# Kernel optimization log

Measured on AMD Instinct MI355X. Metric: run time of the kernel, lower is better.

The kernel has to match this reference:

```python
import jax, jax.numpy as jnp
import numpy as np
from jax import lax

WINDOW_SIZE = 11
SIGMA = 1.5
LEVELS = 5
WEIGHTS = jnp.array([0.0448, 0.2856, 0.3001, 0.2363, 0.1333], dtype=jnp.float32)


def _make_window(ws, channel):
    # 1D gaussian, sigma=1.5, normalized; outer product -> 2D window, tiled per channel
    x = jnp.arange(ws, dtype=jnp.float32) - ws // 2
    g = jnp.exp(-(x * x) / (2.0 * SIGMA * SIGMA))
    g = g / g.sum()
    w2 = jnp.outer(g, g)  # [ws, ws]
    return jnp.broadcast_to(w2[None, None], (channel, 1, ws, ws))


def _dwconv(x, win, channel):
    # depthwise VALID conv, matches F.conv2d(..., padding=0, groups=channel)
    return lax.conv_general_dilated(
        x, win, window_strides=(1, 1), padding='VALID',
        feature_group_count=channel,
        dimension_numbers=('NCHW', 'OIHW', 'NCHW'))


def _ssim_cs(img1, img2):
    # dynamic data range, as in the torch source (L=1 for [0,1) inputs)
    max_val = jnp.where(jnp.max(img1) > 128.0, 255.0, 1.0)
    min_val = jnp.where(jnp.min(img1) < -0.5, -1.0, 0.0)
    L = max_val - min_val

    n, c, h, w = img1.shape
    ws = min(WINDOW_SIZE, h, w)  # static python int
    win = _make_window(ws, c)

    mu1 = _dwconv(img1, win, c)
    mu2 = _dwconv(img2, win, c)
    mu1_sq = mu1 * mu1
    mu2_sq = mu2 * mu2
    mu1_mu2 = mu1 * mu2
    sigma1_sq = _dwconv(img1 * img1, win, c) - mu1_sq
    sigma2_sq = _dwconv(img2 * img2, win, c) - mu2_sq
    sigma12 = _dwconv(img1 * img2, win, c) - mu1_mu2

    C1 = (0.01 * L) ** 2
    C2 = (0.03 * L) ** 2
    v1 = 2.0 * sigma12 + C2
    v2 = sigma1_sq + sigma2_sq + C2
    cs = jnp.mean(v1 / v2)
    ssim_map = (2.0 * mu1_mu2 + C1) * v1 / ((mu1_sq + mu2_sq + C1) * v2)
    return jnp.mean(ssim_map), cs


def _avg_pool2(x):
    # F.avg_pool2d(x, (2,2)): stride 2, no padding (floors odd dims)
    n, c, h, w = x.shape
    x = x[:, :, : (h // 2) * 2, : (w // 2) * 2]
    return x.reshape(n, c, h // 2, 2, w // 2, 2).mean(axis=(3, 5))


def setup_inputs() -> dict:
    key = jax.random.key(0)
    k1, k2 = jax.random.split(key)
    img1 = jax.random.uniform(k1, (16, 3, 512, 512), dtype=jnp.float32)
    img2 = jax.random.uniform(k2, (16, 3, 512, 512), dtype=jnp.float32)
    return {"img1": img1, "img2": img2}


def reference(img1, img2):
    mssim, mcs = [], []
    for _ in range(LEVELS):  # fixed 5-level pyramid, shapes shrink each level
        s, c = _ssim_cs(img1, img2)
        mssim.append(s)
        mcs.append(c)
        img1 = _avg_pool2(img1)
        img2 = _avg_pool2(img2)
    mssim = (jnp.stack(mssim) + 1.0) / 2.0  # normalize=True
    mcs = (jnp.stack(mcs) + 1.0) / 2.0
    pow1 = mcs ** WEIGHTS
    pow2 = mssim ** WEIGHTS
    # NOTE: faithful to source: prod over (pow1[:-1] * pow2[-1]) broadcasts pow2[-1]
    return jnp.prod(pow1[:-1] * pow2[-1])
```

## Files before the change

### kernel.cpp

```cpp
#include <hip/hip_runtime.h>


#define NTHR 512

typedef float v4  __attribute__((ext_vector_type(4)));
typedef float v2f __attribute__((ext_vector_type(2)));

__device__ __forceinline__ float frcp(float x) { return __builtin_amdgcn_rcpf(x); }

#define GW_DEF const float GW[11] = {0.00102840f, 0.00759877f, 0.03600070f, \
    0.10936069f, 0.21300636f, 0.26601172f, 0.21300636f, 0.10936069f,        \
    0.03600070f, 0.00759877f, 0.00102840f};

__device__ __forceinline__ void conv11(const float* s, const float* d,
                                       v4& hs, v4& hd, v4& hss, v4& hdd)
{
    GW_DEF
    #pragma unroll
    for (int j = 0; j < 11; ++j) {
        float w = GW[j];
        v4 sv = {s[j], s[j+1], s[j+2], s[j+3]};
        v4 dv = {d[j], d[j+1], d[j+2], d[j+3]};
        v4 wsv = w * sv, wdv = w * dv;
        hs += wsv; hd += wdv; hss += wsv * sv; hdd += wdv * dv;
    }
}

template<int TROWS>
__device__ void hpass_direct(const float* __restrict__ p1, const float* __restrict__ p2,
                             int H, int tx0, int ty0, v4* hb)
{
    constexpr int HR = TROWS + 10;
    for (int task = threadIdx.x; task < HR * 4; task += NTHR) {
        const int r = task >> 2, cg = task & 3;
        const int gr = ty0 + r;
        const int c0 = tx0 + cg * 8;
        v4 hsA = 0.f, hdA = 0.f, hssA = 0.f, hddA = 0.f;
        v4 hsB = 0.f, hdB = 0.f, hssB = 0.f, hddB = 0.f;
        if (gr < H) {
            float s[20], d[20];
            if (c0 + 20 <= H) {
                const float* pa = p1 + (size_t)gr * H + c0;
                const float* pb = p2 + (size_t)gr * H + c0;
                v4 va0 = *(const v4*)(pa);
                v4 va1 = *(const v4*)(pa + 4);
                v4 va2 = *(const v4*)(pa + 8);
                v4 va3 = *(const v4*)(pa + 12);
                v4 va4 = *(const v4*)(pa + 16);
                v4 vb0 = *(const v4*)(pb);
                v4 vb1 = *(const v4*)(pb + 4);
                v4 vb2 = *(const v4*)(pb + 8);
                v4 vb3 = *(const v4*)(pb + 12);
                v4 vb4 = *(const v4*)(pb + 16);
                v4 sv0 = va0 + vb0, dv0 = va0 - vb0;
                v4 sv1 = va1 + vb1, dv1 = va1 - vb1;
                v4 sv2 = va2 + vb2, dv2 = va2 - vb2;
                v4 sv3 = va3 + vb3, dv3 = va3 - vb3;
                v4 sv4 = va4 + vb4, dv4 = va4 - vb4;
                s[0]=sv0.x; s[1]=sv0.y; s[2]=sv0.z; s[3]=sv0.w;
                s[4]=sv1.x; s[5]=sv1.y; s[6]=sv1.z; s[7]=sv1.w;
                s[8]=sv2.x; s[9]=sv2.y; s[10]=sv2.z; s[11]=sv2.w;
                s[12]=sv3.x; s[13]=sv3.y; s[14]=sv3.z; s[15]=sv3.w;
                s[16]=sv4.x; s[17]=sv4.y; s[18]=sv4.z; s[19]=sv4.w;
                d[0]=dv0.x; d[1]=dv0.y; d[2]=dv0.z; d[3]=dv0.w;
                d[4]=dv1.x; d[5]=dv1.y; d[6]=dv1.z; d[7]=dv1.w;
                d[8]=dv2.x; d[9]=dv2.y; d[10]=dv2.z; d[11]=dv2.w;
                d[12]=dv3.x; d[13]=dv3.y; d[14]=dv3.z; d[15]=dv3.w;
                d[16]=dv4.x; d[17]=dv4.y; d[18]=dv4.z; d[19]=dv4.w;
            } else {
                #pragma unroll
                for (int q = 0; q < 20; ++q) {
                    int cc = c0 + q;
                    float a = (cc < H) ? p1[(size_t)gr * H + cc] : 0.f;
                    float b = (cc < H) ? p2[(size_t)gr * H + cc] : 0.f;
                    s[q] = a + b; d[q] = a - b;
                }
            }
            GW_DEF
            #pragma unroll
            for (int j = 0; j < 11; ++j) {
                float w = GW[j];
                v4 svA = {s[j],   s[j+1], s[j+2], s[j+3]};
                v4 dvA = {d[j],   d[j+1], d[j+2], d[j+3]};
                v4 svB = {s[j+4], s[j+5], s[j+6], s[j+7]};
                v4 dvB = {d[j+4], d[j+5], d[j+6], d[j+7]};
                v4 wsA = w * svA, wdA = w * dvA;
                v4 wsB = w * svB, wdB = w * dvB;
                hsA += wsA; hdA += wdA; hssA += wsA * svA; hddA += wdA * dvA;
                hsB += wsB; hdB += wdB; hssB += wsB * svB; hddB += wdB * dvB;
            }
        }
        v4* row = &hb[r * 33 + cg * 8];
        row[0] = (v4){hsA.x, hdA.x, hssA.x, hddA.x};
        row[1] = (v4){hsA.y, hdA.y, hssA.y, hddA.y};
        row[2] = (v4){hsA.z, hdA.z, hssA.z, hddA.z};
        row[3] = (v4){hsA.w, hdA.w, hssA.w, hddA.w};
        row[4] = (v4){hsB.x, hdB.x, hssB.x, hddB.x};
        row[5] = (v4){hsB.y, hdB.y, hssB.y, hddB.y};
        row[6] = (v4){hsB.z, hdB.z, hssB.z, hddB.z};
        row[7] = (v4){hsB.w, hdB.w, hssB.w, hddB.w};
    }
}

__device__ __forceinline__ float pool2g(const float* __restrict__ sp, int SD, int gr, int cc)
{
    const float* q = sp + (size_t)(4 * gr) * SD + 4 * cc;
    v4 r0 = *(const v4*)q;
    v4 r1 = *(const v4*)(q + SD);
    v4 r2 = *(const v4*)(q + 2 * SD);
    v4 r3 = *(const v4*)(q + 3 * SD);
    float a00 = 0.25f * ((r0.x + r0.y) + (r1.x + r1.y));
    float a01 = 0.25f * ((r0.z + r0.w) + (r1.z + r1.w));
    float a10 = 0.25f * ((r2.x + r2.y) + (r3.x + r3.y));
    float a11 = 0.25f * ((r2.z + r2.w) + (r3.z + r3.w));
    return 0.25f * ((a00 + a01) + (a10 + a11));
}

__device__ __forceinline__ float pool3g(const float* __restrict__ sp, int SD, int gr, int cc)
{
    const float* q = sp + (size_t)(8 * gr) * SD + 8 * cc;
    float p2h[2][2];
    #pragma unroll
    for (int h = 0; h < 2; ++h) {
        const float* qq = q + (size_t)(4 * h) * SD;
        v4 A0 = *(const v4*)qq;
        v4 A1 = *(const v4*)(qq + SD);
        v4 A2 = *(const v4*)(qq + 2 * SD);
        v4 A3 = *(const v4*)(qq + 3 * SD);
        v4 B0 = *(const v4*)(qq + 4);
        v4 B1 = *(const v4*)(qq + SD + 4);
        v4 B2 = *(const v4*)(qq + 2 * SD + 4);
        v4 B3 = *(const v4*)(qq + 3 * SD + 4);
        float p00 = 0.25f * ((A0.x + A0.y) + (A1.x + A1.y));
        float p01 = 0.25f * ((A0.z + A0.w) + (A1.z + A1.w));
        float p10 = 0.25f * ((A2.x + A2.y) + (A3.x + A3.y));
        float p11 = 0.25f * ((A2.z + A2.w) + (A3.z + A3.w));
        float q00 = 0.25f * ((B0.x + B0.y) + (B1.x + B1.y));
        float q01 = 0.25f * ((B0.z + B0.w) + (B1.z + B1.w));
        float q10 = 0.25f * ((B2.x + B2.y) + (B3.x + B3.y));
        float q11 = 0.25f * ((B2.z + B2.w) + (B3.z + B3.w));
        p2h[h][0] = 0.25f * ((p00 + p01) + (p10 + p11));
        p2h[h][1] = 0.25f * ((q00 + q01) + (q10 + q11));
    }
    return 0.25f * ((p2h[0][0] + p2h[0][1]) + (p2h[1][0] + p2h[1][1]));
}

__device__ void stage_x2(const float* __restrict__ s1, const float* __restrict__ s2,
                         int tx0, int ty0, float* la, float* lb)
{
    const int SD = 256, DL = 128;
    for (int t = threadIdx.x; t < 2 * 42 * 22; t += NTHR) {
        int im = t >= 42 * 22; int tt = im ? t - 42 * 22 : t;
        int rr = tt / 22, cp = tt % 22;
        int y = ty0 + rr, x = tx0 + 2 * cp;
        const float* sp = im ? s2 : s1;
        float* lp = im ? lb : la;
        float v0 = 0.f, v1 = 0.f;
        if (y < DL && x < DL) {
            const float* q0 = sp + (size_t)(2 * y) * SD + 2 * x;
            v4 r0 = *(const v4*)q0;
            v4 r1 = *(const v4*)(q0 + SD);
            v0 = 0.25f * ((r0.x + r0.y) + (r1.x + r1.y));
            v1 = 0.25f * ((r0.z + r0.w) + (r1.z + r1.w));
        }
        lp[rr * 45 + 2 * cp]     = v0;
        lp[rr * 45 + 2 * cp + 1] = v1;
    }
}

__device__ void stage_x3(const float* __restrict__ s1, const float* __restrict__ s2,
                         int H, int tx0, int ty0, float* la, float* lb)
{
    const int SD = 4 * H;
    for (int t = threadIdx.x; t < 2 * 26 * 44; t += NTHR) {
        int im = t >= 26 * 44; int tt = im ? t - 26 * 44 : t;
        int rr = tt / 44, cc = tt % 44;
        int y = ty0 + rr, x = tx0 + cc;
        const float* sp = im ? s2 : s1;
        float* lp = im ? lb : la;
        float v = 0.f;
        if (y < H && x < H) v = pool2g(sp, SD, y, x);
        lp[rr * 45 + cc] = v;
    }
}

__device__ void stage_x4(const float* __restrict__ s1, const float* __restrict__ s2,
                         int H, int tx0, int ty0, float* la, float* lb)
{
    const int SD = 8 * H;
    for (int t = threadIdx.x; t < 2 * 26 * 44; t += NTHR) {
        int im = t >= 26 * 44; int tt = im ? t - 26 * 44 : t;
        int rr = tt / 44, cc = tt % 44;
        int y = ty0 + rr, x = tx0 + cc;
        const float* sp = im ? s2 : s1;
        float* lp = im ? lb : la;
        float v = 0.f;
        if (y < H && x < H) v = pool3g(sp, SD, y, x);
        lp[rr * 45 + cc] = v;
    }
}

template<int TROWS>
__device__ void hpass_ldsdir(const float* la, const float* lb,
                             int H, int tx0, int ty0, v4* hb)
{
    constexpr int HR = TROWS + 10;
    (void)tx0;
    for (int task = threadIdx.x; task < HR * 8; task += NTHR) {
        const int r = task >> 3, cg2 = task & 7;
        const int gr = ty0 + r;
        const int c0 = cg2 * 4;
        v4 hs = 0.f, hd = 0.f, hss = 0.f, hdd = 0.f;
        if (gr < H) {
            float s[16], d[16];
            #pragma unroll
            for (int q = 0; q < 16; ++q) {
                float pa = la[r * 45 + c0 + q];
                float pb = lb[r * 45 + c0 + q];
                s[q] = pa + pb; d[q] = pa - pb;
            }
            conv11(s, d, hs, hd, hss, hdd);
        }
        v4* row = &hb[r * 33 + cg2 * 4];
        row[0] = (v4){hs.x, hd.x, hss.x, hdd.x};
        row[1] = (v4){hs.y, hd.y, hss.y, hdd.y};
        row[2] = (v4){hs.z, hd.z, hss.z, hdd.z};
        row[3] = (v4){hs.w, hd.w, hss.w, hdd.w};
    }
}

template<int TROWS>
__device__ void vpass_reduce(int H, int tx0, int ty0, const v4* hb, float* red,
                             float* __restrict__ partS, float* __restrict__ partC)
{
    constexpr int OPT = TROWS * 32 / NTHR;
    constexpr int NW  = NTHR / 64;
    GW_DEF
    const float C1 = 1e-4f, C2 = 9e-4f;
    const int tid   = threadIdx.x;
    const int outHW = H - 10;
    const int col   = tid & 31;
    const int row0  = (tid >> 5) * OPT;
    const float colm = (tx0 + col < outHW) ? 1.f : 0.f;
    v4 A[OPT];
    #pragma unroll
    for (int k = 0; k < OPT; ++k) A[k] = 0.f;

    #pragma unroll
    for (int r = 0; r < OPT + 10; ++r) {
        v4 h = hb[(row0 + r) * 33 + col];
        #pragma unroll
        for (int k = 0; k < OPT; ++k) {
            const int j = r - k;
            if (j >= 0 && j < 11) A[k] += GW[j] * h;
        }
    }

    float ssim_t = 0.f, cs_t = 0.f;
    #pragma unroll
    for (int k = 0; k < OPT; ++k) {
        float mask = colm * ((ty0 + row0 + k < outHW) ? 1.f : 0.f);
        float mu_s = A[k].x, mu_d = A[k].y;
        float P = mu_s * mu_s, Q = mu_d * mu_d;
        float U = A[k].z - P, V = A[k].w - Q;
        float v1 = 0.5f * (U - V) + C2;
        float v2 = 0.5f * (U + V) + C2;
        float n1 = 0.5f * (P - Q) + C1;
        float d1 = 0.5f * (P + Q) + C1;
        float csv = v1 * frcp(v2);
        float ssv = n1 * csv * frcp(d1);
        cs_t   += mask * csv;
        ssim_t += mask * ssv;
    }

    #pragma unroll
    for (int off = 32; off > 0; off >>= 1) {
        ssim_t += __shfl_down(ssim_t, off);
        cs_t   += __shfl_down(cs_t, off);
    }
    int wave = tid >> 6, lane = tid & 63;
    if (lane == 0) { red[wave] = ssim_t; red[NW + wave] = cs_t; }
    __syncthreads();
    if (tid == 0) {
        float s = 0.f, c = 0.f;
        #pragma unroll
        for (int w = 0; w < NW; ++w) { s += red[w]; c += red[NW + w]; }
        partS[0] = s; partC[0] = c;
    }
}

__global__ __launch_bounds__(NTHR, 4) void l0_kernel(
    const float* __restrict__ img1, const float* __restrict__ img2,
    float* __restrict__ x1a, float* __restrict__ x1b,
    float* __restrict__ accS, float* __restrict__ accC)
{
    __shared__ v4 hb[74 * 33];
    __shared__ float red[16];

    const int tid = threadIdx.x;
    const int nc  = blockIdx.z;
    const int tx0 = blockIdx.x * 32;
    const int ty0 = blockIdx.y * 64;
    const int H   = 512;
    const float* p1 = img1 + (size_t)nc * H * H;
    const float* p2 = img2 + (size_t)nc * H * H;

    {
        const int r = tid >> 4, c = tid & 15;
        const int iy = ty0 + 2 * r, ix = tx0 + 2 * c;
        v2f a0 = *(const v2f*)(p1 + (size_t)iy * H + ix);
        v2f a1 = *(const v2f*)(p1 + (size_t)(iy + 1) * H + ix);
        v2f b0 = *(const v2f*)(p2 + (size_t)iy * H + ix);
        v2f b1 = *(const v2f*)(p2 + (size_t)(iy + 1) * H + ix);
        size_t o = (size_t)nc * 256 * 256 + (size_t)((ty0 >> 1) + r) * 256 + ((tx0 >> 1) + c);
        x1a[o] = 0.25f * ((a0.x + a0.y) + (a1.x + a1.y));
        x1b[o] = 0.25f * ((b0.x + b0.y) + (b1.x + b1.y));
    }

    hpass_direct<64>(p1, p2, H, tx0, ty0, hb);
    __syncthreads();
    int fb = (int)blockIdx.x + 16 * ((int)blockIdx.y + 8 * nc);
    vpass_reduce<64>(H, tx0, ty0, hb, red, accS + fb, accC + fb);
}

__global__ __launch_bounds__(NTHR, 4) void tail_kernel(
    const float* __restrict__ x1a, const float* __restrict__ x1b,
    float* __restrict__ accTS, float* __restrict__ accTC)
{
    __shared__ v4 hb[74 * 33];
    __shared__ float red[16];

    const int b = (int)blockIdx.x;
    const size_t X1S = (size_t)256 * 256;

    if (b >= 1248) {
        int lbk = b - 1248;
        int cx = lbk & 7, rem = lbk >> 3, cy = rem & 3, nc = rem >> 2;
        const float* p1 = x1a + (size_t)nc * X1S;
        const float* p2 = x1b + (size_t)nc * X1S;
        int tx0 = cx * 32, ty0 = cy * 64;
        hpass_direct<64>(p1, p2, 256, tx0, ty0, hb);
        __syncthreads();
        vpass_reduce<64>(256, tx0, ty0, hb, red, accTS + b, accTC + b);
    } else if (b >= 480) {
        int lbk = b - 480;
        int cx = lbk & 3, rem = lbk >> 2, cy = rem & 3, nc = rem >> 2;
        const float* p1 = x1a + (size_t)nc * X1S;
        const float* p2 = x1b + (size_t)nc * X1S;
        int tx0 = cx * 32, ty0 = cy * 32;
        float* la = (float*)hb + 5544;
        float* lb = la + 42 * 45;
        stage_x2(p1, p2, tx0, ty0, la, lb);
        __syncthreads();
        hpass_ldsdir<32>(la, lb, 128, tx0, ty0, hb);
        __syncthreads();
        vpass_reduce<32>(128, tx0, ty0, hb, red, accTS + b, accTC + b);
    } else if (b >= 96) {
        int lbk = b - 96;
        int cx = lbk & 1, rem = lbk >> 1, cy = rem & 3, nc = rem >> 2;
        const float* p1 = x1a + (size_t)nc * X1S;
        const float* p2 = x1b + (size_t)nc * X1S;
        int tx0 = cx * 32, ty0 = cy * 16;
        float* la = (float*)hb + 3432;
        float* lb = la + 26 * 45;
        stage_x3(p1, p2, 64, tx0, ty0, la, lb);
        __syncthreads();
        hpass_ldsdir<16>(la, lb, 64, tx0, ty0, hb);
        __syncthreads();
        vpass_reduce<16>(64, tx0, ty0, hb, red, accTS + b, accTC + b);
    } else {
        int cy = b & 1, nc = b >> 1;
        const float* p1 = x1a + (size_t)nc * X1S;
        const float* p2 = x1b + (size_t)nc * X1S;
        int tx0 = 0, ty0 = cy * 16;
        float* la = (float*)hb + 3432;
        float* lb = la + 26 * 45;
        stage_x4(p1, p2, 32, tx0, ty0, la, lb);
        __syncthreads();
        hpass_ldsdir<16>(la, lb, 32, tx0, ty0, hb);
        __syncthreads();
        vpass_reduce<16>(32, tx0, ty0, hb, red, accTS + b, accTC + b);
    }
}

__global__ void finalize_kernel(const float* __restrict__ acc0S, const float* __restrict__ acc0C,
                                const float* __restrict__ accTS, const float* __restrict__ accTC,
                                float* __restrict__ out)
{
    __shared__ float sm[10];
    __shared__ float wred[8];
    const int tid  = (int)threadIdx.x;
    const int wave = tid >> 6, lane = tid & 63;
    const int st[5] = {0, 1248, 480, 96, 0};
    const int en[5] = {6144, 2784, 1248, 480, 96};

    for (int srs = 0; srs < 10; ++srs) {
        int l = srs >> 1;
        float p = 0.f;
        if (l == 0) {
            const float* base = (srs & 1) ? acc0C : acc0S;
            for (int i = tid; i < 6144; i += NTHR) p += base[i];
        } else {
            const float* base = (srs & 1) ? accTC : accTS;
            for (int i = st[l] + tid; i < en[l]; i += NTHR) p += base[i];
        }
        #pragma unroll
        for (int o = 32; o > 0; o >>= 1) p += __shfl_down(p, o);
        if (lane == 0) wred[wave] = p;
        __syncthreads();
        if (tid == 0) {
            float t = 0.f;
            #pragma unroll
            for (int w = 0; w < 8; ++w) t += wred[w];
            sm[srs] = t;
        }
        __syncthreads();
    }

    if (tid == 0) {
        const float w[5] = {0.0448f, 0.2856f, 0.3001f, 0.2363f, 0.1333f};
        float ms[5], mc[5];
        for (int l = 0; l < 5; ++l) {
            int oh = (512 >> l) - 10;
            float cnt = 48.f * (float)oh * (float)oh;
            ms[l] = (sm[2 * l] / cnt + 1.f) * 0.5f;
            mc[l] = (sm[2 * l + 1] / cnt + 1.f) * 0.5f;
        }
        float p2 = powf(ms[4], w[4]);
        float r = 1.f;
        for (int i = 0; i < 4; ++i) r *= powf(mc[i], w[i]) * p2;
        out[0] = r;
    }
}

extern "C" void kernel_launch(void* const* d_in, const int* in_sizes, int n_in,
                              void* d_out, int out_size, void* d_ws, size_t ws_size,
                              hipStream_t stream)
{
    (void)in_sizes; (void)n_in; (void)out_size; (void)ws_size;
    const float* img1 = (const float*)d_in[0];
    const float* img2 = (const float*)d_in[1];
    float* out = (float*)d_out;
    float* ws  = (float*)d_ws;

    float* acc0S = ws;
    float* acc0C = acc0S + 6144;
    float* accTS = acc0C + 6144;
    float* accTC = accTS + 2784;
    float* x1a   = accTC + 2784;
    float* x1b   = x1a + (size_t)48 * 256 * 256;

    l0_kernel<<<dim3(16, 8, 48), NTHR, 0, stream>>>(
        img1, img2, x1a, x1b, acc0S, acc0C);
    tail_kernel<<<dim3(2784), NTHR, 0, stream>>>(
        x1a, x1b, accTS, accTC);
    finalize_kernel<<<1, NTHR, 0, stream>>>(
        acc0S, acc0C, accTS, accTC, out);
}
```

Baseline: 216.7 us.

## Compute pyramid level 1 in the level-0 kernel by pooling on the fly

Level-1 SSIM tiles now run as extra blocks in the first kernel. Each of these blocks pools the original 512x512 images into shared memory itself instead of reading the pooled buffer written by a previous kernel. This takes level 1 off the tail kernel's serial path and lets it overlap with level-0 work. The cost is re-reading and re-pooling the full-resolution inputs for level 1. The accumulator buffers are merged into one contiguous layout, and the finalize index ranges are updated to match.

```diff
diff --git a/kernel.cpp b/kernel.cpp
--- a/kernel.cpp
+++ b/kernel.cpp
@@ -145,10 +145,9 @@
     return 0.25f * ((p2h[0][0] + p2h[0][1]) + (p2h[1][0] + p2h[1][1]));
 }
 
-__device__ void stage_x2(const float* __restrict__ s1, const float* __restrict__ s2,
-                         int tx0, int ty0, float* la, float* lb)
-{
-    const int SD = 256, DL = 128;
+__device__ void stage_pool1g(const float* __restrict__ s1, const float* __restrict__ s2,
+                             int SD, int DL, int tx0, int ty0, float* la, float* lb)
+{
     for (int t = threadIdx.x; t < 2 * 42 * 22; t += NTHR) {
         int im = t >= 42 * 22; int tt = im ? t - 42 * 22 : t;
         int rr = tt / 22, cp = tt % 22;
@@ -289,7 +288,7 @@
     }
 }
 
-__global__ __launch_bounds__(NTHR, 4) void l0_kernel(
+__global__ __launch_bounds__(NTHR, 4) void main_kernel(
     const float* __restrict__ img1, const float* __restrict__ img2,
     float* __restrict__ x1a, float* __restrict__ x1b,
     float* __restrict__ accS, float* __restrict__ accC)
@@ -297,52 +296,58 @@
     __shared__ v4 hb[74 * 33];
     __shared__ float red[16];
 
+    const int b   = (int)blockIdx.x;
     const int tid = threadIdx.x;
-    const int nc  = blockIdx.z;
-    const int tx0 = blockIdx.x * 32;
-    const int ty0 = blockIdx.y * 64;
-    const int H   = 512;
-    const float* p1 = img1 + (size_t)nc * H * H;
-    const float* p2 = img2 + (size_t)nc * H * H;
-
-    {
-        const int r = tid >> 4, c = tid & 15;
-        const int iy = ty0 + 2 * r, ix = tx0 + 2 * c;
-        v2f a0 = *(const v2f*)(p1 + (size_t)iy * H + ix);
-        v2f a1 = *(const v2f*)(p1 + (size_t)(iy + 1) * H + ix);
-        v2f b0 = *(const v2f*)(p2 + (size_t)iy * H + ix);
-        v2f b1 = *(const v2f*)(p2 + (size_t)(iy + 1) * H + ix);
-        size_t o = (size_t)nc * 256 * 256 + (size_t)((ty0 >> 1) + r) * 256 + ((tx0 >> 1) + c);
-        x1a[o] = 0.25f * ((a0.x + a0.y) + (a1.x + a1.y));
-        x1b[o] = 0.25f * ((b0.x + b0.y) + (b1.x + b1.y));
-    }
-
-    hpass_direct<64>(p1, p2, H, tx0, ty0, hb);
-    __syncthreads();
-    int fb = (int)blockIdx.x + 16 * ((int)blockIdx.y + 8 * nc);
-    vpass_reduce<64>(H, tx0, ty0, hb, red, accS + fb, accC + fb);
-}
-
-__global__ __launch_bounds__(NTHR, 4) void tail_kernel(
+    const size_t IMS = (size_t)512 * 512;
+
+    if (b < 6144) {
+        int cx = b & 15, rem = b >> 4, cy = rem & 7, nc = rem >> 3;
+        const float* p1 = img1 + (size_t)nc * IMS;
+        const float* p2 = img2 + (size_t)nc * IMS;
+        int tx0 = cx * 32, ty0 = cy * 64;
+        {
+            const int r = tid >> 4, c = tid & 15;
+            const int iy = ty0 + 2 * r, ix = tx0 + 2 * c;
+            v2f a0 = *(const v2f*)(p1 + (size_t)iy * 512 + ix);
+            v2f a1 = *(const v2f*)(p1 + (size_t)(iy + 1) * 512 + ix);
+            v2f b0 = *(const v2f*)(p2 + (size_t)iy * 512 + ix);
+            v2f b1 = *(const v2f*)(p2 + (size_t)(iy + 1) * 512 + ix);
+            size_t o = (size_t)nc * 256 * 256 + (size_t)((ty0 >> 1) + r) * 256 + ((tx0 >> 1) + c);
+            x1a[o] = 0.25f * ((a0.x + a0.y) + (a1.x + a1.y));
+            x1b[o] = 0.25f * ((b0.x + b0.y) + (b1.x + b1.y));
+        }
+        hpass_direct<64>(p1, p2, 512, tx0, ty0, hb);
+        __syncthreads();
+        vpass_reduce<64>(512, tx0, ty0, hb, red, accS + b, accC + b);
+    } else {
+        int lbk = b - 6144;
+        int cx = lbk & 7, rem = lbk >> 3, cy = rem & 7, nc = rem >> 3;
+        const float* p1 = img1 + (size_t)nc * IMS;
+        const float* p2 = img2 + (size_t)nc * IMS;
+        int tx0 = cx * 32, ty0 = cy * 32;
+        float* la = (float*)hb + 5544;
+        float* lb = la + 42 * 45;
+        stage_pool1g(p1, p2, 512, 256, tx0, ty0, la, lb);
+        __syncthreads();
+        hpass_ldsdir<32>(la, lb, 256, tx0, ty0, hb);
+        __syncthreads();
+        vpass_reduce<32>(256, tx0, ty0, hb, red, accS + b, accC + b);
+    }
+}
+
+__global__ __launch_bounds__(NTHR, 4) void deep_kernel(
     const float* __restrict__ x1a, const float* __restrict__ x1b,
-    float* __restrict__ accTS, float* __restrict__ accTC)
+    float* __restrict__ accS, float* __restrict__ accC)
 {
     __shared__ v4 hb[74 * 33];
     __shared__ float red[16];
 
     const int b = (int)blockIdx.x;
     const size_t X1S = (size_t)256 * 256;
-
-    if (b >= 1248) {
-        int lbk = b - 1248;
-        int cx = lbk & 7, rem = lbk >> 3, cy = rem & 3, nc = rem >> 2;
-        const float* p1 = x1a + (size_t)nc * X1S;
-        const float* p2 = x1b + (size_t)nc * X1S;
-        int tx0 = cx * 32, ty0 = cy * 64;
-        hpass_direct<64>(p1, p2, 256, tx0, ty0, hb);
-        __syncthreads();
-        vpass_reduce<64>(256, tx0, ty0, hb, red, accTS + b, accTC + b);
-    } else if (b >= 480) {
+    float* pS = accS + 9216 + b;
+    float* pC = accC + 9216 + b;
+
+    if (b >= 480) {
         int lbk = b - 480;
         int cx = lbk & 3, rem = lbk >> 2, cy = rem & 3, nc = rem >> 2;
         const float* p1 = x1a + (size_t)nc * X1S;
@@ -350,11 +355,11 @@
         int tx0 = cx * 32, ty0 = cy * 32;
         float* la = (float*)hb + 5544;
         float* lb = la + 42 * 45;
-        stage_x2(p1, p2, tx0, ty0, la, lb);
+        stage_pool1g(p1, p2, 256, 128, tx0, ty0, la, lb);
         __syncthreads();
         hpass_ldsdir<32>(la, lb, 128, tx0, ty0, hb);
         __syncthreads();
-        vpass_reduce<32>(128, tx0, ty0, hb, red, accTS + b, accTC + b);
+        vpass_reduce<32>(128, tx0, ty0, hb, red, pS, pC);
     } else if (b >= 96) {
         int lbk = b - 96;
         int cx = lbk & 1, rem = lbk >> 1, cy = rem & 3, nc = rem >> 2;
@@ -367,7 +372,7 @@
         __syncthreads();
         hpass_ldsdir<16>(la, lb, 64, tx0, ty0, hb);
         __syncthreads();
-        vpass_reduce<16>(64, tx0, ty0, hb, red, accTS + b, accTC + b);
+        vpass_reduce<16>(64, tx0, ty0, hb, red, pS, pC);
     } else {
         int cy = b & 1, nc = b >> 1;
         const float* p1 = x1a + (size_t)nc * X1S;
@@ -379,31 +384,25 @@
         __syncthreads();
         hpass_ldsdir<16>(la, lb, 32, tx0, ty0, hb);
         __syncthreads();
-        vpass_reduce<16>(32, tx0, ty0, hb, red, accTS + b, accTC + b);
-    }
-}
-
-__global__ void finalize_kernel(const float* __restrict__ acc0S, const float* __restrict__ acc0C,
-                                const float* __restrict__ accTS, const float* __restrict__ accTC,
+        vpass_reduce<16>(32, tx0, ty0, hb, red, pS, pC);
+    }
+}
+
+__global__ void finalize_kernel(const float* __restrict__ accS, const float* __restrict__ accC,
                                 float* __restrict__ out)
 {
     __shared__ float sm[10];
     __shared__ float wred[8];
     const int tid  = (int)threadIdx.x;
     const int wave = tid >> 6, lane = tid & 63;
-    const int st[5] = {0, 1248, 480, 96, 0};
-    const int en[5] = {6144, 2784, 1248, 480, 96};
+    const int st[5] = {0, 6144, 9696, 9312, 9216};
+    const int en[5] = {6144, 9216, 10464, 9696, 9312};
 
     for (int srs = 0; srs < 10; ++srs) {
         int l = srs >> 1;
+        const float* base = (srs & 1) ? accC : accS;
         float p = 0.f;
-        if (l == 0) {
-            const float* base = (srs & 1) ? acc0C : acc0S;
-            for (int i = tid; i < 6144; i += NTHR) p += base[i];
-        } else {
-            const float* base = (srs & 1) ? accTC : accTS;
-            for (int i = st[l] + tid; i < en[l]; i += NTHR) p += base[i];
-        }
+        for (int i = st[l] + tid; i < en[l]; i += NTHR) p += base[i];
         #pragma unroll
         for (int o = 32; o > 0; o >>= 1) p += __shfl_down(p, o);
         if (lane == 0) wred[wave] = p;
@@ -443,17 +442,14 @@
     float* out = (float*)d_out;
     float* ws  = (float*)d_ws;
 
-    float* acc0S = ws;
-    float* acc0C = acc0S + 6144;
-    float* accTS = acc0C + 6144;
-    float* accTC = accTS + 2784;
-    float* x1a   = accTC + 2784;
-    float* x1b   = x1a + (size_t)48 * 256 * 256;
-
-    l0_kernel<<<dim3(16, 8, 48), NTHR, 0, stream>>>(
-        img1, img2, x1a, x1b, acc0S, acc0C);
-    tail_kernel<<<dim3(2784), NTHR, 0, stream>>>(
-        x1a, x1b, accTS, accTC);
-    finalize_kernel<<<1, NTHR, 0, stream>>>(
-        acc0S, acc0C, accTS, accTC, out);
-}
+    float* accS = ws;
+    float* accC = accS + 10464;
+    float* x1a  = accC + 10464;
+    float* x1b  = x1a + (size_t)48 * 256 * 256;
+
+    main_kernel<<<dim3(9216), NTHR, 0, stream>>>(
+        img1, img2, x1a, x1b, accS, accC);
+    deep_kernel<<<dim3(1248), NTHR, 0, stream>>>(
+        x1a, x1b, accS, accC);
+    finalize_kernel<<<1, NTHR, 0, stream>>>(accS, accC, out);
+}
```

Measured after the change: 222.8 us. 2.8% more time.
